# Performance work log

Hardware: AMD Instinct MI355X
Metric: run time of the kernel (lower is better)

## Reference

```python
import jax, jax.numpy as jnp
import numpy as np

N = 50000      # nodes in batched graph
E = 1600000    # edges (avg degree ~32)
D = 64         # feature width (features_dim = h_dim = out_dim)
R = 4          # num_rels (bond types)
L = 4          # RGCN layers: i2h + 2 hidden + h2o
B = 256        # graphs in the batch
NEG_SLOPE = 0.2


def setup_inputs() -> dict:
    key = jax.random.key(0)
    ks = jax.random.split(key, 12)
    h = jax.random.normal(ks[0], (N, D), jnp.float32)
    src = jax.random.randint(ks[1], (E,), 0, N, jnp.int32)
    dst = jax.random.randint(ks[2], (E,), 0, N, jnp.int32)
    etypes = jax.random.randint(ks[3], (E,), 0, R, jnp.int32)
    gids = jnp.sort(jax.random.randint(ks[4], (N,), 0, B, jnp.int32))
    Wrel = jax.random.normal(ks[5], (L, R, D, D), jnp.float32) * 0.05
    Wloop = jax.random.normal(ks[6], (L, D, D), jnp.float32) * 0.05
    brel = jnp.zeros((L, D), jnp.float32)
    Wg = jax.random.normal(ks[7], (D, D), jnp.float32) * 0.05
    al = jax.random.normal(ks[8], (D,), jnp.float32) * 0.05
    ar = jax.random.normal(ks[9], (D,), jnp.float32) * 0.05
    Wd = jax.random.normal(ks[10], (D, 1), jnp.float32) * 0.05
    bd = jnp.zeros((1,), jnp.float32)
    return dict(h=h, Wrel=Wrel, Wloop=Wloop, brel=brel, Wg=Wg, al=al, ar=ar,
                Wd=Wd, bd=bd, src=src, dst=dst, etypes=etypes, gids=gids)


def reference(h, Wrel, Wloop, brel, Wg, al, ar, Wd, bd, src, dst, etypes, gids):
    n = h.shape[0]
    # --- stacked RelGraphConv layers (basis regularizer with num_bases=num_rels
    # -> per-relation weight), self-loop + bias + ReLU, sum aggregation ---
    for l in range(Wrel.shape[0]):
        hr = jnp.einsum('nd,rdo->nro', h, Wrel[l])          # [N, R, D]
        msg = hr[src, etypes]                                # [E, D] gather
        agg = jax.ops.segment_sum(msg, dst, num_segments=n)  # [N, D] scatter-add
        h = jax.nn.relu(agg + h @ Wloop[l] + brel[l])
    # --- GATConv, 1 head ---
    z = h @ Wg                                               # [N, D]
    el = z @ al                                              # [N] a_l . z
    er = z @ ar                                              # [N] a_r . z
    e = jax.nn.leaky_relu(el[src] + er[dst], NEG_SLOPE)      # [E]
    m = jax.ops.segment_max(e, dst, num_segments=n)          # edge-softmax (stable)
    ex = jnp.exp(e - m[dst])
    den = jax.ops.segment_sum(ex, dst, num_segments=n)
    alpha = ex / jnp.maximum(den[dst], 1e-9)                 # [E]
    hg = jax.ops.segment_sum(alpha[:, None] * z[src], dst, num_segments=n)  # [N, D]
    # --- SumPooling over each graph, view [N,1,D] -> pooled [B,1,D] ---
    pooled = jax.ops.segment_sum(hg, gids, num_segments=B)[:, None, :]
    # --- dense head ---
    return pooled @ Wd + bd                                  # [B, 1, 1]
```

## Files before the change

### kernel.cpp

```cpp
#include <hip/hip_runtime.h>

#define DD 64
#define EPB 1024
#define NREP 8

typedef float f32x4 __attribute__((ext_vector_type(4)));
typedef __bf16 bf16x8 __attribute__((ext_vector_type(8)));

__device__ __forceinline__ unsigned enc_f32(float x) {
  unsigned u = __float_as_uint(x);
  return (u & 0x80000000u) ? ~u : (u | 0x80000000u);
}
__device__ __forceinline__ float dec_f32(unsigned k) {
  return (k & 0x80000000u) ? __uint_as_float(k ^ 0x80000000u)
                           : __uint_as_float(~k);
}
__device__ __forceinline__ unsigned f2bf(float x) {
  unsigned u = __float_as_uint(x);
  return (u + 0x7fffu + ((u >> 16) & 1u)) >> 16;
}
__device__ __forceinline__ void unpack8(const uint4 raw, float* v) {
  v[0] = __uint_as_float(raw.x << 16);
  v[1] = __uint_as_float(raw.x & 0xffff0000u);
  v[2] = __uint_as_float(raw.y << 16);
  v[3] = __uint_as_float(raw.y & 0xffff0000u);
  v[4] = __uint_as_float(raw.z << 16);
  v[5] = __uint_as_float(raw.z & 0xffff0000u);
  v[6] = __uint_as_float(raw.w << 16);
  v[7] = __uint_as_float(raw.w & 0xffff0000u);
}
__device__ __forceinline__ float4 unpack4(const uint2 r) {
  return make_float4(__uint_as_float(r.x << 16),
                     __uint_as_float(r.x & 0xffff0000u),
                     __uint_as_float(r.y << 16),
                     __uint_as_float(r.y & 0xffff0000u));
}
__device__ __forceinline__ bf16x8 as_bf16x8(uint4 u) {
  union {
    uint4 u;
    bf16x8 b;
  } cv;
  cv.u = u;
  return cv.b;
}

__global__ __launch_bounds__(256) void conv_bf16(const float* __restrict__ x,
                                                 ushort* __restrict__ xb,
                                                 int n4) {
  int i = blockIdx.x * 256 + threadIdx.x;
  if (i < n4) {
    float4 v = ((const float4*)x)[i];
    uint2 o;
    o.x = f2bf(v.x) | (f2bf(v.y) << 16);
    o.y = f2bf(v.z) | (f2bf(v.w) << 16);
    ((uint2*)xb)[i] = o;
  }
}

__global__ __launch_bounds__(256) void f2_coarse(
    const int* __restrict__ src, const int* __restrict__ dst,
    const int* __restrict__ et, int* __restrict__ gcur,
    unsigned* __restrict__ staging, int E) {
  __shared__ int lcnt[256];
  __shared__ int sc[256];
  __shared__ int lbase[256];
  __shared__ int gb[256];
  __shared__ unsigned rec[EPB];
  __shared__ unsigned char rbk[EPB];

  const int t = threadIdx.x;
  const int base = blockIdx.x * EPB;
  const int rep = blockIdx.x & (NREP - 1);
  const int bc = min(EPB, E - base);

  lcnt[t] = 0;
  __syncthreads();

  int d_[EPB / 256], se_[EPB / 256], rk_[EPB / 256];
#pragma unroll
  for (int k = 0; k < EPB / 256; ++k) {
    const int e = base + k * 256 + t;
    if (e < E) {
      const int d = dst[e];
      d_[k] = d;
      se_[k] = (src[e] << 2) | et[e];
      rk_[k] = atomicAdd(&lcnt[d >> 8], 1);
    } else {
      d_[k] = -1;
    }
  }
  __syncthreads();

  const int lv = lcnt[t];
  sc[t] = lv;
  __syncthreads();
#pragma unroll
  for (int off = 1; off < 256; off <<= 1) {
    const int add = (t >= off) ? sc[t - off] : 0;
    __syncthreads();
    sc[t] += add;
    __syncthreads();
  }
  lbase[t] = sc[t] - lv;
  gb[t] = lv ? atomicAdd(&gcur[rep * 256 + t], lv) : 0;
  __syncthreads();

#pragma unroll
  for (int k = 0; k < EPB / 256; ++k) {
    if (d_[k] >= 0) {
      const int cb = d_[k] >> 8;
      const int pos = lbase[cb] + rk_[k];
      rec[pos] = ((unsigned)(d_[k] & 255) << 24) | (unsigned)se_[k];
      rbk[pos] = (unsigned char)cb;
    }
  }
  __syncthreads();

  for (int idx = t; idx < bc; idx += 256) {
    const int cb = rbk[idx];
    staging[gb[cb] + (idx - lbase[cb])] = rec[idx];
  }
}

__global__ __launch_bounds__(256) void cscan2(const int* __restrict__ gcur,
                                              int* __restrict__ cbase,
                                              int* __restrict__ rowptr, int N,
                                              int E, int CAP, int CAP8) {
  __shared__ int s[256];
  const int t = threadIdx.x;
  int c = 0;
#pragma unroll
  for (int r = 0; r < NREP; ++r)
    c += gcur[r * 256 + t] - (t * CAP + r * CAP8);
  s[t] = c;
  __syncthreads();
#pragma unroll
  for (int off = 1; off < 256; off <<= 1) {
    const int add = (t >= off) ? s[t - off] : 0;
    __syncthreads();
    s[t] += add;
    __syncthreads();
  }
  cbase[t] = s[t] - c;
  if (t == 0) rowptr[N] = E;
}

__global__ __launch_bounds__(256) void f3_fine4(
    const unsigned* __restrict__ staging, const int* __restrict__ gcur,
    const int* __restrict__ cbase, int* __restrict__ rowptr,
    int* __restrict__ srcet, int N, int CAP, int CAP8) {
  __shared__ int hist[256];
  __shared__ int sc[256];
  __shared__ int lcur[256];
  __shared__ int before;
  const int cb = blockIdx.x >> 2;
  const int sub = blockIdx.x & 3;
  const int t = threadIdx.x;
  const int dlo = sub << 6;

  hist[t] = 0;
  if (t == 0) before = 0;
  __syncthreads();

  int myb = 0;
#pragma unroll 1
  for (int r = 0; r < NREP; ++r) {
    const int s0 = cb * CAP + r * CAP8;
    const int s1 = gcur[r * 256 + cb];
    for (int i = s0 + t; i < s1; i += 256) {
      const unsigned rc = staging[i];
      const int dl = (int)(rc >> 24);
      const int off = dl - dlo;
      if ((unsigned)off < 64u)
        atomicAdd(&hist[(off << 2) | (int)(rc & 3u)], 1);
      else if (dl < dlo)
        ++myb;
    }
  }
#pragma unroll
  for (int off = 32; off > 0; off >>= 1) myb += __shfl_down(myb, off);
  if ((t & 63) == 0 && myb) atomicAdd(&before, myb);
  __syncthreads();

  const int v = hist[t];
  sc[t] = v;
  __syncthreads();
#pragma unroll
  for (int off = 1; off < 256; off <<= 1) {
    const int add = (t >= off) ? sc[t - off] : 0;
    __syncthreads();
    sc[t] += add;
    __syncthreads();
  }
  const int base = cbase[cb] + before + sc[t] - v;
  lcur[t] = base;
  if ((t & 3) == 0) {
    const int dn = (cb << 8) + dlo + (t >> 2);
    if (dn < N) rowptr[dn] = base;
  }
  __syncthreads();

#pragma unroll 1
  for (int r = 0; r < NREP; ++r) {
    const int s0 = cb * CAP + r * CAP8;
    const int s1 = gcur[r * 256 + cb];
    for (int i = s0 + t; i < s1; i += 256) {
      const unsigned rc = staging[i];
      const int dl = (int)(rc >> 24);
      const int off = dl - dlo;
      if ((unsigned)off < 64u) {
        const int pos = atomicAdd(&lcur[(off << 2) | (int)(rc & 3u)], 1);
        srcet[pos] = (int)(rc & 0xFFFFFFu);
      }
    }
  }
}

#define ACCUM(se, v)                                                         \
  {                                                                          \
    const int r_ = (se) & 3;                                                 \
    if (r_ == 0) { a0.x += v.x; a0.y += v.y; a0.z += v.z; a0.w += v.w; }     \
    else if (r_ == 1) { a1.x += v.x; a1.y += v.y; a1.z += v.z; a1.w += v.w; }\
    else if (r_ == 2) { a2.x += v.x; a2.y += v.y; a2.z += v.z; a2.w += v.w; }\
    else { a3.x += v.x; a3.y += v.y; a3.z += v.z; a3.w += v.w; }             \
  }

__global__ __launch_bounds__(256) void gather_rel(
    const ushort* __restrict__ hb, const int* __restrict__ rowptr,
    const int* __restrict__ srcet, ushort* __restrict__ aggr_bf, int N) {
  const int n = blockIdx.x * 4 + (threadIdx.x >> 6);
  const int lane = threadIdx.x & 63;
  const int g = lane >> 4;
  const int t = lane & 15;
  if (n >= N) return;
  const int beg = rowptr[n], end = rowptr[n + 1];

  float4 a0 = make_float4(0.f, 0.f, 0.f, 0.f);
  float4 a1 = a0, a2 = a0, a3 = a0;

  int j = beg + g;
  for (; j + 28 < end; j += 32) {
    const int se0 = srcet[j];
    const int se1 = srcet[j + 4];
    const int se2 = srcet[j + 8];
    const int se3 = srcet[j + 12];
    const int se4 = srcet[j + 16];
    const int se5 = srcet[j + 20];
    const int se6 = srcet[j + 24];
    const int se7 = srcet[j + 28];
    const uint2 r0 = *(const uint2*)(hb + ((size_t)(se0 >> 2) << 6) + (t << 2));
    const uint2 r1 = *(const uint2*)(hb + ((size_t)(se1 >> 2) << 6) + (t << 2));
    const uint2 r2 = *(const uint2*)(hb + ((size_t)(se2 >> 2) << 6) + (t << 2));
    const uint2 r3 = *(const uint2*)(hb + ((size_t)(se3 >> 2) << 6) + (t << 2));
    const uint2 r4 = *(const uint2*)(hb + ((size_t)(se4 >> 2) << 6) + (t << 2));
    const uint2 r5 = *(const uint2*)(hb + ((size_t)(se5 >> 2) << 6) + (t << 2));
    const uint2 r6 = *(const uint2*)(hb + ((size_t)(se6 >> 2) << 6) + (t << 2));
    const uint2 r7 = *(const uint2*)(hb + ((size_t)(se7 >> 2) << 6) + (t << 2));
    const float4 v0 = unpack4(r0);
    const float4 v1 = unpack4(r1);
    const float4 v2 = unpack4(r2);
    const float4 v3 = unpack4(r3);
    const float4 v4 = unpack4(r4);
    const float4 v5 = unpack4(r5);
    const float4 v6 = unpack4(r6);
    const float4 v7 = unpack4(r7);
    ACCUM(se0, v0);
    ACCUM(se1, v1);
    ACCUM(se2, v2);
    ACCUM(se3, v3);
    ACCUM(se4, v4);
    ACCUM(se5, v5);
    ACCUM(se6, v6);
    ACCUM(se7, v7);
  }
  for (; j + 12 < end; j += 16) {
    const int se0 = srcet[j];
    const int se1 = srcet[j + 4];
    const int se2 = srcet[j + 8];
    const int se3 = srcet[j + 12];
    const uint2 r0 = *(const uint2*)(hb + ((size_t)(se0 >> 2) << 6) + (t << 2));
    const uint2 r1 = *(const uint2*)(hb + ((size_t)(se1 >> 2) << 6) + (t << 2));
    const uint2 r2 = *(const uint2*)(hb + ((size_t)(se2 >> 2) << 6) + (t << 2));
    const uint2 r3 = *(const uint2*)(hb + ((size_t)(se3 >> 2) << 6) + (t << 2));
    const float4 v0 = unpack4(r0);
    const float4 v1 = unpack4(r1);
    const float4 v2 = unpack4(r2);
    const float4 v3 = unpack4(r3);
    ACCUM(se0, v0);
    ACCUM(se1, v1);
    ACCUM(se2, v2);
    ACCUM(se3, v3);
  }
  for (; j < end; j += 4) {
    const int se0 = srcet[j];
    const uint2 r0 = *(const uint2*)(hb + ((size_t)(se0 >> 2) << 6) + (t << 2));
    const float4 v0 = unpack4(r0);
    ACCUM(se0, v0);
  }

#pragma unroll
  for (int off = 16; off <= 32; off <<= 1) {
    a0.x += __shfl_xor(a0.x, off); a0.y += __shfl_xor(a0.y, off);
    a0.z += __shfl_xor(a0.z, off); a0.w += __shfl_xor(a0.w, off);
    a1.x += __shfl_xor(a1.x, off); a1.y += __shfl_xor(a1.y, off);
    a1.z += __shfl_xor(a1.z, off); a1.w += __shfl_xor(a1.w, off);
    a2.x += __shfl_xor(a2.x, off); a2.y += __shfl_xor(a2.y, off);
    a2.z += __shfl_xor(a2.z, off); a2.w += __shfl_xor(a2.w, off);
    a3.x += __shfl_xor(a3.x, off); a3.y += __shfl_xor(a3.y, off);
    a3.z += __shfl_xor(a3.z, off); a3.w += __shfl_xor(a3.w, off);
  }

  const float4 res = (g == 0) ? a0 : (g == 1) ? a1 : (g == 2) ? a2 : a3;
  uint2 p;
  p.x = f2bf(res.x) | (f2bf(res.y) << 16);
  p.y = f2bf(res.z) | (f2bf(res.w) << 16);
  *(uint2*)(aggr_bf + ((size_t)n << 8) + (g << 6) + (t << 2)) = p;
}

__global__ __launch_bounds__(256) void pack_w(
    const float* __restrict__ Wrel, const float* __restrict__ Wloop,
    const float* __restrict__ Wg, const float* __restrict__ al,
    const float* __restrict__ ar, const float* __restrict__ Wd,
    ushort* __restrict__ wpk, float* __restrict__ vav, int L) {
  const int l = blockIdx.x;
  if (l < L) {
    for (int f = threadIdx.x; f < 2560; f += 256) {
      const int lane = f & 63;
      const int kc = f >> 6;
      const int kt = kc >> 2;
      const int c = kc & 3;
      const int o = c * 16 + (lane & 15);
      const int kl0 = (lane >> 4) * 8;
      const float* wsrc =
          (kt < 8)
              ? Wrel + ((((size_t)l * 4 + (kt >> 1)) * 64 + (kt & 1) * 32 + kl0) * 64)
              : Wloop + (((size_t)l * 64 + (kt - 8) * 32 + kl0) * 64);
      unsigned o8[8];
#pragma unroll
      for (int j = 0; j < 8; ++j) o8[j] = f2bf(wsrc[(size_t)j * 64 + o]);
      uint4 p;
      p.x = o8[0] | (o8[1] << 16);
      p.y = o8[2] | (o8[3] << 16);
      p.z = o8[4] | (o8[5] << 16);
      p.w = o8[6] | (o8[7] << 16);
      *(uint4*)(wpk + (size_t)l * 20480 + (size_t)f * 8) = p;
    }
  } else {
    const int tt = threadIdx.x;
    if (tt < 192) {
      const int which = tt >> 6;
      const int d = tt & 63;
      const float* v = (which == 0) ? al : (which == 1) ? ar : Wd;
      float s = 0.f;
#pragma unroll
      for (int o = 0; o < 64; ++o) s = fmaf(Wg[d * 64 + o], v[o], s);
      vav[tt] = s;
    }
  }
}

__global__ __launch_bounds__(256) void rgcn_dense_mfma(
    const ushort* __restrict__ aggr_bf, const ushort* __restrict__ hb_in,
    const ushort* __restrict__ wpk, const float* __restrict__ bias,
    ushort* __restrict__ hb_out, int N) {
  __shared__ __align__(16) char smraw[40960];
  const int tid = threadIdx.x;

  {
    const uint4* gsrc = (const uint4*)wpk;
    uint4* ldst = (uint4*)smraw;
#pragma unroll
    for (int i = 0; i < 10; ++i) ldst[i * 256 + tid] = gsrc[i * 256 + tid];
  }

  const int w = tid >> 6;
  const int lane = tid & 63;
  const int t = lane & 15;
  const int g = lane >> 4;
  const int n = blockIdx.x * 64 + w * 16 + t;
  const bool valid = n < N;

  f32x4 acc[4];
#pragma unroll
  for (int c = 0; c < 4; ++c) {
    const float b = bias[c * 16 + t];
    f32x4 z = {b, b, b, b};
    acc[c] = z;
  }

  __syncthreads();
  const bf16x8* bfr = (const bf16x8*)smraw;

#pragma unroll
  for (int kt = 0; kt < 10; ++kt) {
    uint4 raw = make_uint4(0u, 0u, 0u, 0u);
    if (valid) {
      const ushort* ap =
          (kt < 8) ? aggr_bf + (((size_t)n) << 8) + (kt << 5) + (g << 3)
                   : hb_in + (((size_t)n) << 6) + ((kt - 8) << 5) + (g << 3);
      raw = *(const uint4*)ap;
    }
    const bf16x8 a = as_bf16x8(raw);
#pragma unroll
    for (int c = 0; c < 4; ++c) {
      acc[c] = __builtin_amdgcn_mfma_f32_16x16x32_bf16(
          a, bfr[(kt * 4 + c) * 64 + lane], acc[c], 0, 0, 0);
    }
  }

  __syncthreads();
  float* tile = (float*)smraw;
  {
    const int r0 = w * 16 + g * 4;
#pragma unroll
    for (int c = 0; c < 4; ++c) {
      const int col = c * 16 + t;
#pragma unroll
      for (int r = 0; r < 4; ++r)
        tile[(r0 + r) * 65 + col] = fmaxf(acc[c][r], 0.f);
    }
  }
  __syncthreads();
  const int n0 = blockIdx.x * 64;
#pragma unroll
  for (int q = 0; q < 2; ++q) {
    const int f = q * 256 + tid;
    const int row = f >> 3;
    const int c8 = (f & 7) << 3;
    const int nn = n0 + row;
    if (nn < N) {
      const float* s = tile + row * 65 + c8;
      uint4 p;
      p.x = f2bf(s[0]) | (f2bf(s[1]) << 16);
      p.y = f2bf(s[2]) | (f2bf(s[3]) << 16);
      p.z = f2bf(s[4]) | (f2bf(s[5]) << 16);
      p.w = f2bf(s[6]) | (f2bf(s[7]) << 16);
      *(uint4*)(hb_out + (((size_t)nn) << 6) + c8) = p;
    }
  }
}

__global__ __launch_bounds__(256) void gat_proj(
    const ushort* __restrict__ hb, const float* __restrict__ vav,
    float2* __restrict__ ely, float* __restrict__ er,
    unsigned* __restrict__ genc, int N) {
  __shared__ float sv[192];
  const int tid = threadIdx.x;
  if (tid < 192) sv[tid] = vav[tid];
  __syncthreads();
  const int n = blockIdx.x * 256 + tid;
  float pl = 0.f, pr = 0.f, py = 0.f;
  if (n < N) {
    const ushort* row = hb + ((size_t)n << 6);
#pragma unroll
    for (int q = 0; q < 8; ++q) {
      const uint4 raw = *(const uint4*)(row + (q << 3));
      float v[8];
      unpack8(raw, v);
#pragma unroll
      for (int j = 0; j < 8; ++j) {
        pl = fmaf(v[j], sv[q * 8 + j], pl);
        pr = fmaf(v[j], sv[64 + q * 8 + j], pr);
        py = fmaf(v[j], sv[128 + q * 8 + j], py);
      }
    }
    ely[n] = make_float2(pl, py);
    er[n] = pr;
  }
  float mx = (n < N) ? pl : -1e30f;
#pragma unroll
  for (int off = 32; off > 0; off >>= 1) mx = fmaxf(mx, __shfl_xor(mx, off));
  if ((tid & 63) == 0) atomicMax(genc, enc_f32(mx));
}

#define GSC_NPG 2
#define GSC_NPB (16 * GSC_NPG)
__global__ __launch_bounds__(256) void gat_scalar(
    const float2* __restrict__ ely, const float* __restrict__ er,
    const int* __restrict__ rowptr, const int* __restrict__ srcet,
    const unsigned* __restrict__ genc, const int* __restrict__ gids,
    float* __restrict__ out, int N, int B) {
  __shared__ float acc[256];
  for (int i = threadIdx.x; i < B; i += 256) acc[i] = 0.f;
  __syncthreads();
  const int grp = threadIdx.x >> 4;
  const int ln = threadIdx.x & 15;
  const float gmax = dec_f32(*genc);
  const int base = blockIdx.x * GSC_NPB + grp * GSC_NPG;

#pragma unroll
  for (int i = 0; i < GSC_NPG; ++i) {
    const int n = base + i;
    if (n < N) {
      const int beg = rowptr[n], end = rowptr[n + 1];
      const float ern = er[n];
      float mb = gmax + ern;
      mb = (mb > 0.f) ? mb : 0.2f * mb;
      float num = 0.f, den = 0.f;
      for (int j = beg + ln; j < end; j += 16) {
        const float2 e2 = ely[srcet[j] >> 2];
        float x = e2.x + ern;
        x = (x > 0.f) ? x : 0.2f * x;
        const float w = __expf(x - mb);
        num = fmaf(w, e2.y, num);
        den += w;
      }
#pragma unroll
      for (int off = 1; off < 16; off <<= 1) {
        num += __shfl_xor(num, off);
        den += __shfl_xor(den, off);
      }
      if (ln == 0) atomicAdd(&acc[gids[n]], num / fmaxf(den, 1e-9f));
    }
  }
  __syncthreads();
  for (int i = threadIdx.x; i < B; i += 256) {
    const float v = acc[i];
    if (v != 0.f) unsafeAtomicAdd(out + i, v);
  }
}

__global__ void init_out_k(float* out, const float* bd, int n, unsigned* genc,
                           int* gcur, int CAP, int CAP8) {
  int i = blockIdx.x * blockDim.x + threadIdx.x;
  if (i < n) out[i] = bd[0];
  if (i < 256 * NREP) {
    const int r = i >> 8;
    const int b = i & 255;
    gcur[i] = b * CAP + r * CAP8;
  }
  if (i == 0) *genc = enc_f32(-1e30f);
}

extern "C" void kernel_launch(void* const* d_in, const int* in_sizes, int n_in,
                              void* d_out, int out_size, void* d_ws,
                              size_t ws_size, hipStream_t stream) {
  const float* h0 = (const float*)d_in[0];
  const float* Wrel = (const float*)d_in[1];
  const float* Wloop = (const float*)d_in[2];
  const float* brel = (const float*)d_in[3];
  const float* Wg = (const float*)d_in[4];
  const float* al = (const float*)d_in[5];
  const float* ar = (const float*)d_in[6];
  const float* Wd = (const float*)d_in[7];
  const float* bd = (const float*)d_in[8];
  const int* src = (const int*)d_in[9];
  const int* dst = (const int*)d_in[10];
  const int* et = (const int*)d_in[11];
  const int* gids = (const int*)d_in[12];

  const int N = in_sizes[0] / DD;
  const int E = in_sizes[9];
  const int L = in_sizes[2] / (DD * DD);
  float* out = (float*)d_out;
  const int CAP8 = ((E / (256 * NREP)) * 2 + 63) & ~63;
  const int CAP = CAP8 * NREP;

  char* wsb = (char*)d_ws;
  ushort* hbA = (ushort*)wsb;
  ushort* hbB = hbA + (size_t)N * DD;
  ushort* aggr_bf = hbB + (size_t)N * DD;
  int* rowptr = (int*)(aggr_bf + (size_t)N * 256);
  int* srcet = rowptr + N + 1;
  float2* ely = (float2*)(srcet + E);
  float* er = (float*)(ely + N);
  int* gcur = (int*)(er + N);
  int* cbase = gcur + 256 * NREP;
  unsigned* genc = (unsigned*)(cbase + 256);
  unsigned* staging = (unsigned*)aggr_bf;
  float* vav = (float*)(genc + 1);
  ushort* wpk = (ushort*)(((size_t)(char*)ely + 15) & ~(size_t)15);

  dim3 b256(256);
  const int grid_dense = (N + 63) / 64;
  const int nfb = (E + EPB - 1) / EPB;
  const int ncb = (N + 255) >> 8;

  hipLaunchKernelGGL(init_out_k, dim3((max(out_size, 256 * NREP) + 255) / 256),
                     b256, 0, stream, out, bd, out_size, genc, gcur, CAP, CAP8);

  hipLaunchKernelGGL(pack_w, dim3(L + 1), b256, 0, stream, Wrel, Wloop, Wg, al,
                     ar, Wd, wpk, vav, L);

  hipLaunchKernelGGL(f2_coarse, dim3(nfb), b256, 0, stream, src, dst, et, gcur,
                     staging, E);
  hipLaunchKernelGGL(cscan2, dim3(1), b256, 0, stream, gcur, cbase, rowptr, N,
                     E, CAP, CAP8);
  hipLaunchKernelGGL(f3_fine4, dim3(ncb * 4), b256, 0, stream, staging, gcur,
                     cbase, rowptr, srcet, N, CAP, CAP8);

  hipLaunchKernelGGL(conv_bf16, dim3((N * DD / 4 + 255) / 256), b256, 0, stream,
                     h0, hbA, N * DD / 4);

  ushort* cur = hbA;
  ushort* nxt = hbB;
  for (int l = 0; l < L; ++l) {
    hipLaunchKernelGGL(gather_rel, dim3((N + 3) / 4), b256, 0, stream, cur,
                       rowptr, srcet, aggr_bf, N);
    hipLaunchKernelGGL(rgcn_dense_mfma, dim3(grid_dense), b256, 0, stream,
                       aggr_bf, cur, wpk + (size_t)l * 20480,
                       brel + (size_t)l * DD, nxt, N);
    ushort* tmp = cur; cur = nxt; nxt = tmp;
  }

  hipLaunchKernelGGL(gat_proj, dim3((N + 255) / 256), b256, 0, stream, cur, vav,
                     ely, er, genc, N);
  const int grid_gs = (N + GSC_NPB - 1) / GSC_NPB;
  hipLaunchKernelGGL(gat_scalar, dim3(grid_gs), b256, 0, stream, ely, er,
                     rowptr, srcet, genc, gids, out, N, out_size);
}
```

Before: 361.8 us.

## Widen gather_rel to 16-byte loads and fold init/convert kernels into others

gather_rel now has 8 lanes per edge, each loading a uint4 (8 bf16 values), so 8 edges are processed in parallel per wave instead of 4. Each lane holds 8-wide accumulators and the shuffle reduction gains one extra step. Separately, the init_out and conv_bf16 kernels are removed: their work moves into extra blocks of pack_w and f2_coarse, which saves two launches. Having 8 edge groups but only 4 relation outputs means only half the lanes store results, and register pressure rises from the larger accumulators.

```diff
diff --git a/kernel.cpp b/kernel.cpp
--- a/kernel.cpp
+++ b/kernel.cpp
@@ -5,6 +5,7 @@
 #define NREP 8
 
 typedef float f32x4 __attribute__((ext_vector_type(4)));
+typedef float f32x8 __attribute__((ext_vector_type(8)));
 typedef __bf16 bf16x8 __attribute__((ext_vector_type(8)));
 
 __device__ __forceinline__ unsigned enc_f32(float x) {
@@ -29,11 +30,17 @@
   v[6] = __uint_as_float(raw.w << 16);
   v[7] = __uint_as_float(raw.w & 0xffff0000u);
 }
-__device__ __forceinline__ float4 unpack4(const uint2 r) {
-  return make_float4(__uint_as_float(r.x << 16),
-                     __uint_as_float(r.x & 0xffff0000u),
-                     __uint_as_float(r.y << 16),
-                     __uint_as_float(r.y & 0xffff0000u));
+__device__ __forceinline__ f32x8 unpack8v(const uint4 r) {
+  f32x8 v;
+  v[0] = __uint_as_float(r.x << 16);
+  v[1] = __uint_as_float(r.x & 0xffff0000u);
+  v[2] = __uint_as_float(r.y << 16);
+  v[3] = __uint_as_float(r.y & 0xffff0000u);
+  v[4] = __uint_as_float(r.z << 16);
+  v[5] = __uint_as_float(r.z & 0xffff0000u);
+  v[6] = __uint_as_float(r.w << 16);
+  v[7] = __uint_as_float(r.w & 0xffff0000u);
+  return v;
 }
 __device__ __forceinline__ bf16x8 as_bf16x8(uint4 u) {
   union {
@@ -44,23 +51,11 @@
   return cv.b;
 }
 
-__global__ __launch_bounds__(256) void conv_bf16(const float* __restrict__ x,
-                                                 ushort* __restrict__ xb,
-                                                 int n4) {
-  int i = blockIdx.x * 256 + threadIdx.x;
-  if (i < n4) {
-    float4 v = ((const float4*)x)[i];
-    uint2 o;
-    o.x = f2bf(v.x) | (f2bf(v.y) << 16);
-    o.y = f2bf(v.z) | (f2bf(v.w) << 16);
-    ((uint2*)xb)[i] = o;
-  }
-}
-
 __global__ __launch_bounds__(256) void f2_coarse(
     const int* __restrict__ src, const int* __restrict__ dst,
     const int* __restrict__ et, int* __restrict__ gcur,
-    unsigned* __restrict__ staging, int E) {
+    unsigned* __restrict__ staging, int E, int nfb,
+    const float* __restrict__ h0, ushort* __restrict__ hbA, int n4) {
   __shared__ int lcnt[256];
   __shared__ int sc[256];
   __shared__ int lbase[256];
@@ -69,6 +64,19 @@
   __shared__ unsigned char rbk[EPB];
 
   const int t = threadIdx.x;
+
+  if (blockIdx.x >= nfb) {
+    const int i = (blockIdx.x - nfb) * 256 + t;
+    if (i < n4) {
+      float4 v = ((const float4*)h0)[i];
+      uint2 o;
+      o.x = f2bf(v.x) | (f2bf(v.y) << 16);
+      o.y = f2bf(v.z) | (f2bf(v.w) << 16);
+      ((uint2*)hbA)[i] = o;
+    }
+    return;
+  }
+
   const int base = blockIdx.x * EPB;
   const int rep = blockIdx.x & (NREP - 1);
   const int bc = min(EPB, E - base);
@@ -216,13 +224,21 @@
   }
 }
 
-#define ACCUM(se, v)                                                         \
+#define ACCUM8(se, v)                                                        \
   {                                                                          \
     const int r_ = (se) & 3;                                                 \
-    if (r_ == 0) { a0.x += v.x; a0.y += v.y; a0.z += v.z; a0.w += v.w; }     \
-    else if (r_ == 1) { a1.x += v.x; a1.y += v.y; a1.z += v.z; a1.w += v.w; }\
-    else if (r_ == 2) { a2.x += v.x; a2.y += v.y; a2.z += v.z; a2.w += v.w; }\
-    else { a3.x += v.x; a3.y += v.y; a3.z += v.z; a3.w += v.w; }             \
+    if (r_ == 0) aA += (v);                                                  \
+    else if (r_ == 1) aB += (v);                                             \
+    else if (r_ == 2) aC += (v);                                             \
+    else aD += (v);                                                          \
+  }
+
+#define RED8(a)                                                              \
+  {                                                                          \
+    a[0] += __shfl_xor(a[0], off); a[1] += __shfl_xor(a[1], off);            \
+    a[2] += __shfl_xor(a[2], off); a[3] += __shfl_xor(a[3], off);            \
+    a[4] += __shfl_xor(a[4], off); a[5] += __shfl_xor(a[5], off);            \
+    a[6] += __shfl_xor(a[6], off); a[7] += __shfl_xor(a[7], off);            \
   }
 
 __global__ __launch_bounds__(256) void gather_rel(
@@ -230,98 +246,66 @@
     const int* __restrict__ srcet, ushort* __restrict__ aggr_bf, int N) {
   const int n = blockIdx.x * 4 + (threadIdx.x >> 6);
   const int lane = threadIdx.x & 63;
-  const int g = lane >> 4;
-  const int t = lane & 15;
+  const int g = lane >> 3;
+  const int t = lane & 7;
   if (n >= N) return;
   const int beg = rowptr[n], end = rowptr[n + 1];
 
-  float4 a0 = make_float4(0.f, 0.f, 0.f, 0.f);
-  float4 a1 = a0, a2 = a0, a3 = a0;
+  f32x8 aA = {0.f, 0.f, 0.f, 0.f, 0.f, 0.f, 0.f, 0.f};
+  f32x8 aB = aA, aC = aA, aD = aA;
 
   int j = beg + g;
-  for (; j + 28 < end; j += 32) {
+  for (; j + 24 < end; j += 32) {
     const int se0 = srcet[j];
-    const int se1 = srcet[j + 4];
-    const int se2 = srcet[j + 8];
-    const int se3 = srcet[j + 12];
-    const int se4 = srcet[j + 16];
-    const int se5 = srcet[j + 20];
-    const int se6 = srcet[j + 24];
-    const int se7 = srcet[j + 28];
-    const uint2 r0 = *(const uint2*)(hb + ((size_t)(se0 >> 2) << 6) + (t << 2));
-    const uint2 r1 = *(const uint2*)(hb + ((size_t)(se1 >> 2) << 6) + (t << 2));
-    const uint2 r2 = *(const uint2*)(hb + ((size_t)(se2 >> 2) << 6) + (t << 2));
-    const uint2 r3 = *(const uint2*)(hb + ((size_t)(se3 >> 2) << 6) + (t << 2));
-    const uint2 r4 = *(const uint2*)(hb + ((size_t)(se4 >> 2) << 6) + (t << 2));
-    const uint2 r5 = *(const uint2*)(hb + ((size_t)(se5 >> 2) << 6) + (t << 2));
-    const uint2 r6 = *(const uint2*)(hb + ((size_t)(se6 >> 2) << 6) + (t << 2));
-    const uint2 r7 = *(const uint2*)(hb + ((size_t)(se7 >> 2) << 6) + (t << 2));
-    const float4 v0 = unpack4(r0);
-    const float4 v1 = unpack4(r1);
-    const float4 v2 = unpack4(r2);
-    const float4 v3 = unpack4(r3);
-    const float4 v4 = unpack4(r4);
-    const float4 v5 = unpack4(r5);
-    const float4 v6 = unpack4(r6);
-    const float4 v7 = unpack4(r7);
-    ACCUM(se0, v0);
-    ACCUM(se1, v1);
-    ACCUM(se2, v2);
-    ACCUM(se3, v3);
-    ACCUM(se4, v4);
-    ACCUM(se5, v5);
-    ACCUM(se6, v6);
-    ACCUM(se7, v7);
-  }
-  for (; j + 12 < end; j += 16) {
+    const int se1 = srcet[j + 8];
+    const int se2 = srcet[j + 16];
+    const int se3 = srcet[j + 24];
+    const uint4 r0 = *(const uint4*)(hb + ((size_t)(se0 >> 2) << 6) + (t << 3));
+    const uint4 r1 = *(const uint4*)(hb + ((size_t)(se1 >> 2) << 6) + (t << 3));
+    const uint4 r2 = *(const uint4*)(hb + ((size_t)(se2 >> 2) << 6) + (t << 3));
+    const uint4 r3 = *(const uint4*)(hb + ((size_t)(se3 >> 2) << 6) + (t << 3));
+    const f32x8 v0 = unpack8v(r0);
+    const f32x8 v1 = unpack8v(r1);
+    const f32x8 v2 = unpack8v(r2);
+    const f32x8 v3 = unpack8v(r3);
+    ACCUM8(se0, v0);
+    ACCUM8(se1, v1);
+    ACCUM8(se2, v2);
+    ACCUM8(se3, v3);
+  }
+  for (; j < end; j += 8) {
     const int se0 = srcet[j];
-    const int se1 = srcet[j + 4];
-    const int se2 = srcet[j + 8];
-    const int se3 = srcet[j + 12];
-    const uint2 r0 = *(const uint2*)(hb + ((size_t)(se0 >> 2) << 6) + (t << 2));
-    const uint2 r1 = *(const uint2*)(hb + ((size_t)(se1 >> 2) << 6) + (t << 2));
-    const uint2 r2 = *(const uint2*)(hb + ((size_t)(se2 >> 2) << 6) + (t << 2));
-    const uint2 r3 = *(const uint2*)(hb + ((size_t)(se3 >> 2) << 6) + (t << 2));
-    const float4 v0 = unpack4(r0);
-    const float4 v1 = unpack4(r1);
-    const float4 v2 = unpack4(r2);
-    const float4 v3 = unpack4(r3);
-    ACCUM(se0, v0);
-    ACCUM(se1, v1);
-    ACCUM(se2, v2);
-    ACCUM(se3, v3);
-  }
-  for (; j < end; j += 4) {
-    const int se0 = srcet[j];
-    const uint2 r0 = *(const uint2*)(hb + ((size_t)(se0 >> 2) << 6) + (t << 2));
-    const float4 v0 = unpack4(r0);
-    ACCUM(se0, v0);
-  }
-
-#pragma unroll
-  for (int off = 16; off <= 32; off <<= 1) {
-    a0.x += __shfl_xor(a0.x, off); a0.y += __shfl_xor(a0.y, off);
-    a0.z += __shfl_xor(a0.z, off); a0.w += __shfl_xor(a0.w, off);
-    a1.x += __shfl_xor(a1.x, off); a1.y += __shfl_xor(a1.y, off);
-    a1.z += __shfl_xor(a1.z, off); a1.w += __shfl_xor(a1.w, off);
-    a2.x += __shfl_xor(a2.x, off); a2.y += __shfl_xor(a2.y, off);
-    a2.z += __shfl_xor(a2.z, off); a2.w += __shfl_xor(a2.w, off);
-    a3.x += __shfl_xor(a3.x, off); a3.y += __shfl_xor(a3.y, off);
-    a3.z += __shfl_xor(a3.z, off); a3.w += __shfl_xor(a3.w, off);
-  }
-
-  const float4 res = (g == 0) ? a0 : (g == 1) ? a1 : (g == 2) ? a2 : a3;
-  uint2 p;
-  p.x = f2bf(res.x) | (f2bf(res.y) << 16);
-  p.y = f2bf(res.z) | (f2bf(res.w) << 16);
-  *(uint2*)(aggr_bf + ((size_t)n << 8) + (g << 6) + (t << 2)) = p;
+    const uint4 r0 = *(const uint4*)(hb + ((size_t)(se0 >> 2) << 6) + (t << 3));
+    const f32x8 v0 = unpack8v(r0);
+    ACCUM8(se0, v0);
+  }
+
+#pragma unroll
+  for (int off = 8; off <= 32; off <<= 1) {
+    RED8(aA);
+    RED8(aB);
+    RED8(aC);
+    RED8(aD);
+  }
+
+  if (g < 4) {
+    const f32x8 res = (g == 0) ? aA : (g == 1) ? aB : (g == 2) ? aC : aD;
+    uint4 p;
+    p.x = f2bf(res[0]) | (f2bf(res[1]) << 16);
+    p.y = f2bf(res[2]) | (f2bf(res[3]) << 16);
+    p.z = f2bf(res[4]) | (f2bf(res[5]) << 16);
+    p.w = f2bf(res[6]) | (f2bf(res[7]) << 16);
+    *(uint4*)(aggr_bf + ((size_t)n << 8) + (g << 6) + (t << 3)) = p;
+  }
 }
 
 __global__ __launch_bounds__(256) void pack_w(
     const float* __restrict__ Wrel, const float* __restrict__ Wloop,
     const float* __restrict__ Wg, const float* __restrict__ al,
     const float* __restrict__ ar, const float* __restrict__ Wd,
-    ushort* __restrict__ wpk, float* __restrict__ vav, int L) {
+    ushort* __restrict__ wpk, float* __restrict__ vav, int L,
+    float* __restrict__ out, const float* __restrict__ bd, int out_n,
+    unsigned* __restrict__ genc, int* __restrict__ gcur, int CAP, int CAP8) {
   const int l = blockIdx.x;
   if (l < L) {
     for (int f = threadIdx.x; f < 2560; f += 256) {
@@ -345,7 +329,7 @@
       p.w = o8[6] | (o8[7] << 16);
       *(uint4*)(wpk + (size_t)l * 20480 + (size_t)f * 8) = p;
     }
-  } else {
+  } else if (l == L) {
     const int tt = threadIdx.x;
     if (tt < 192) {
       const int which = tt >> 6;
@@ -356,6 +340,15 @@
       for (int o = 0; o < 64; ++o) s = fmaf(Wg[d * 64 + o], v[o], s);
       vav[tt] = s;
     }
+  } else {
+    const int tt = threadIdx.x;
+    for (int i = tt; i < out_n; i += 256) out[i] = bd[0];
+    for (int i = tt; i < 256 * NREP; i += 256) {
+      const int r = i >> 8;
+      const int b = i & 255;
+      gcur[i] = b * CAP + r * CAP8;
+    }
+    if (tt == 0) *genc = enc_f32(-1e30f);
   }
 }
 
@@ -520,18 +513,6 @@
   }
 }
 
-__global__ void init_out_k(float* out, const float* bd, int n, unsigned* genc,
-                           int* gcur, int CAP, int CAP8) {
-  int i = blockIdx.x * blockDim.x + threadIdx.x;
-  if (i < n) out[i] = bd[0];
-  if (i < 256 * NREP) {
-    const int r = i >> 8;
-    const int b = i & 255;
-    gcur[i] = b * CAP + r * CAP8;
-  }
-  if (i == 0) *genc = enc_f32(-1e30f);
-}
-
 extern "C" void kernel_launch(void* const* d_in, const int* in_sizes, int n_in,
                               void* d_out, int out_size, void* d_ws,
                               size_t ws_size, hipStream_t stream) {
@@ -575,22 +556,19 @@
   const int grid_dense = (N + 63) / 64;
   const int nfb = (E + EPB - 1) / EPB;
   const int ncb = (N + 255) >> 8;
-
-  hipLaunchKernelGGL(init_out_k, dim3((max(out_size, 256 * NREP) + 255) / 256),
-                     b256, 0, stream, out, bd, out_size, genc, gcur, CAP, CAP8);
-
-  hipLaunchKernelGGL(pack_w, dim3(L + 1), b256, 0, stream, Wrel, Wloop, Wg, al,
-                     ar, Wd, wpk, vav, L);
-
-  hipLaunchKernelGGL(f2_coarse, dim3(nfb), b256, 0, stream, src, dst, et, gcur,
-                     staging, E);
+  const int n4 = N * DD / 4;
+  const int ncv = (n4 + 255) / 256;
+
+  hipLaunchKernelGGL(pack_w, dim3(L + 2), b256, 0, stream, Wrel, Wloop, Wg, al,
+                     ar, Wd, wpk, vav, L, out, bd, out_size, genc, gcur, CAP,
+                     CAP8);
+
+  hipLaunchKernelGGL(f2_coarse, dim3(nfb + ncv), b256, 0, stream, src, dst, et,
+                     gcur, staging, E, nfb, h0, hbA, n4);
   hipLaunchKernelGGL(cscan2, dim3(1), b256, 0, stream, gcur, cbase, rowptr, N,
                      E, CAP, CAP8);
   hipLaunchKernelGGL(f3_fine4, dim3(ncb * 4), b256, 0, stream, staging, gcur,
                      cbase, rowptr, srcet, N, CAP, CAP8);
-
-  hipLaunchKernelGGL(conv_bf16, dim3((N * DD / 4 + 255) / 256), b256, 0, stream,
-                     h0, hbA, N * DD / 4);
 
   ushort* cur = hbA;
   ushort* nxt = hbB;
```

After: 417.7 us. 15.5% more time.
